# Kernel tuning notes

Measured on AMD Instinct MI355X. Metric: run time of the kernel, lower is better.

The kernel has to match this reference:

```python
import jax, jax.numpy as jnp
import numpy as np

UPDATE_STEPS = 2
EPS = 1e-7


def _collect(attn, source, W, b):
    """_Collection_Unit: relu(Linear(source)) gathered by attention, row-averaged.
    attn: [N_tgt, N_src], source: [N_src, D_in], W: [D_out, D_in], b: [D_out]."""
    fc_out = jax.nn.relu(source @ W.T + b)          # [N_src, D_out]
    collect = attn @ fc_out                          # [N_tgt, D_out]
    denom = jnp.sum(attn, axis=1, keepdims=True) + EPS
    return collect / denom


def setup_inputs() -> dict:
    key = jax.random.key(0)
    ks = jax.random.split(key, 10)
    N_OBJ, N_REL, D = 2048, 16384, 1024
    inp = {
        "obj_feats": jax.random.normal(ks[0], (N_OBJ, D), jnp.float32),
        "rel_feats": jax.random.normal(ks[1], (N_REL, D), jnp.float32),
        "attn_sub": jax.random.uniform(ks[2], (N_OBJ, N_REL), jnp.float32),
        "attn_obj": jax.random.uniform(ks[3], (N_OBJ, N_REL), jnp.float32),
        "attn_self": jax.random.uniform(ks[4], (N_OBJ, N_OBJ), jnp.float32),
    }
    # normal_init(fc, 0, 0.01) per original module
    names = ["rel2obj_sub", "rel2obj_obj", "obj2rel_sub", "obj2rel_obj", "obj2obj"]
    for i, n in enumerate(names):
        inp[f"W_{n}"] = jax.random.normal(ks[5 + i], (D, D), jnp.float32) * 0.01
        inp[f"b_{n}"] = jnp.zeros((D,), jnp.float32)
    return inp


def reference(obj_feats, rel_feats, attn_sub, attn_obj, attn_self,
              W_rel2obj_sub, b_rel2obj_sub, W_rel2obj_obj, b_rel2obj_obj,
              W_obj2rel_sub, b_obj2rel_sub, W_obj2rel_obj, b_obj2rel_obj,
              W_obj2obj, b_obj2obj):
    x_obj, x_rel = obj_feats, rel_feats
    for _ in range(UPDATE_STEPS):
        # collect to objects: from relations (as subject / as object) and from other objects
        src_sub = _collect(attn_sub, x_rel, W_rel2obj_sub, b_rel2obj_sub)   # unit 0
        src_obj = _collect(attn_obj, x_rel, W_rel2obj_obj, b_rel2obj_obj)   # unit 1
        src_self = _collect(attn_self, x_obj, W_obj2obj, b_obj2obj)         # unit 4
        src2obj = (src_sub + src_obj + src_self) / 3.0
        x_obj_new = x_obj + src2obj                                          # _Update_Unit 0
        # collect to relations: from subject / object node features
        src_rel_sub = _collect(attn_sub.T, x_obj, W_obj2rel_sub, b_obj2rel_sub)  # unit 2
        src_rel_obj = _collect(attn_obj.T, x_obj, W_obj2rel_obj, b_obj2rel_obj)  # unit 3
        src2rel = (src_rel_sub + src_rel_obj) / 2.0
        x_rel = x_rel + src2rel                                              # _Update_Unit 1
        x_obj = x_obj_new
    return x_obj, x_rel
```

## Files before the change

### kernel.cpp

```cpp
#include <hip/hip_runtime.h>
#include <hip/hip_bf16.h>

typedef __attribute__((ext_vector_type(4))) float  f32x4;
typedef __attribute__((ext_vector_type(8))) __bf16 bf16x8;
typedef __attribute__((ext_vector_type(4))) int    i32x4;
typedef __attribute__((ext_vector_type(8))) int    i32x8;
typedef __hip_bfloat16 bf16_t;

#define GT 256
#define BM 128
#define BN 128
#define BK 32

#define NOBJ 2048
#define NREL 16384
#define DIM  1024
#define KOBJ 34816
#define KREL 4096

#define AS1Q __attribute__((address_space(1)))
#define AS3Q __attribute__((address_space(3)))

__device__ __forceinline__ void gload_lds16(const void* g, void* l) {
    __builtin_amdgcn_global_load_lds((AS1Q void*)const_cast<void*>(g),
                                     (AS3Q void*)l, 16, 0, 0);
}

#define MFMA_BF16 __builtin_amdgcn_mfma_f32_16x16x32_bf16
#define MFMA_F8(ACC, Af, Bf) \
    ACC = __builtin_amdgcn_mfma_scale_f32_16x16x128_f8f6f4( \
        Af, Bf, ACC, 0, 0, 0, 0x7F7F7F7F, 0, 0x7F7F7F7F)

#define VMCNT(N) asm volatile("s_waitcnt vmcnt(" #N ")" ::: "memory")
#define SBAR()   __builtin_amdgcn_sched_barrier(0)

__device__ __forceinline__ unsigned char fp8_byte(float x) {
    return (unsigned char)(__builtin_amdgcn_cvt_pk_fp8_f32(x, x, 0, false) & 0xFF);
}
__device__ __forceinline__ unsigned pk4_fp8(float a, float b, float c, float d) {
    int v = __builtin_amdgcn_cvt_pk_fp8_f32(a, b, 0, false);
    v = __builtin_amdgcn_cvt_pk_fp8_f32(c, d, v, true);
    return (unsigned)v;
}

__global__ __launch_bounds__(GT)
void gemm_bt_f234(const bf16_t* __restrict__ A, const bf16_t* __restrict__ B,
                  int M, int N, int K, const float* __restrict__ vecM,
                  unsigned char* __restrict__ fcRel8, unsigned char* __restrict__ fcObj8)
{
    __shared__ bf16_t sA[BM * BK];
    __shared__ bf16_t sB[BN * BK];

    const int tid  = threadIdx.x;
    const int lane = tid & 63;
    const int wid  = tid >> 6;
    const int wr = wid >> 1, wc = wid & 1;
    const int l15 = lane & 15, lk = lane >> 4;

    const long rowA0 = (long)blockIdx.x * BM;
    const long rowB0 = (long)blockIdx.y * BN;
    const long ldab  = (long)K * 2;

    const int c0 = tid, c1 = tid + GT;
    const int r0c = c0 >> 2, k0c = (c0 & 3) ^ ((r0c >> 1) & 3);
    const int r1c = c1 >> 2, k1c = (c1 & 3) ^ ((r1c >> 1) & 3);

    const char* gA0 = (const char*)A + (rowA0 + r0c) * ldab + k0c * 16;
    const char* gA1 = (const char*)A + (rowA0 + r1c) * ldab + k1c * 16;
    const char* gB0 = (const char*)B + (rowB0 + r0c) * ldab + k0c * 16;
    const char* gB1 = (const char*)B + (rowB0 + r1c) * ldab + k1c * 16;
    char* lA0 = (char*)sA + c0 * 16;
    char* lA1 = (char*)sA + c1 * 16;
    char* lB0 = (char*)sB + c0 * 16;
    char* lB1 = (char*)sB + c1 * 16;

    f32x4 acc[4][4];
    #pragma unroll
    for (int i = 0; i < 4; i++)
        #pragma unroll
        for (int j = 0; j < 4; j++) acc[i][j] = f32x4{0.f, 0.f, 0.f, 0.f};

    const int ktPer = K / BK;
    for (int kt = 0; kt < ktPer; ++kt) {
        const long kByte = (long)kt * (BK * 2);
        gload_lds16(gA0 + kByte, lA0);
        gload_lds16(gA1 + kByte, lA1);
        gload_lds16(gB0 + kByte, lB0);
        gload_lds16(gB1 + kByte, lB1);
        __syncthreads();

        bf16x8 af[4], bg[4];
        #pragma unroll
        for (int i = 0; i < 4; i++) {
            const int rr = wr * 64 + i * 16 + l15;
            const int kk = lk ^ ((rr >> 1) & 3);
            af[i] = *reinterpret_cast<const bf16x8*>((const char*)sA + rr * 64 + kk * 16);
        }
        #pragma unroll
        for (int j = 0; j < 4; j++) {
            const int rr = wc * 64 + j * 16 + l15;
            const int kk = lk ^ ((rr >> 1) & 3);
            bg[j] = *reinterpret_cast<const bf16x8*>((const char*)sB + rr * 64 + kk * 16);
        }
        #pragma unroll
        for (int i = 0; i < 4; i++)
            #pragma unroll
            for (int j = 0; j < 4; j++)
                acc[i][j] = MFMA_BF16(af[i], bg[j], acc[i][j], 0, 0, 0);
        __syncthreads();
    }

    #pragma unroll
    for (int i = 0; i < 4; i++) {
        const long mBase = rowA0 + wr * 64 + i * 16 + lk * 4;
        const f32x4 vm = *reinterpret_cast<const f32x4*>(&vecM[mBase]);
        #pragma unroll
        for (int r = 0; r < 4; r++) {
            const long m = mBase + r;
            #pragma unroll
            for (int j = 0; j < 4; j++) {
                const long n = rowB0 + wc * 64 + j * 16 + l15;
                const float v = fmaxf(acc[i][j][r] + vm[r], 0.f);
                const unsigned char o = fp8_byte(v);
                if (m < 1024)            fcRel8[m * (long)KREL + n] = o;
                else if (m < 2048)       fcRel8[(m - 1024) * (long)KREL + 2048 + n] = o;
                else                     fcObj8[(m - 2048) * (long)KOBJ + 32768 + n] = o;
            }
        }
    }
}

__global__ __launch_bounds__(512, 2)
void gemm256fc(const bf16_t* __restrict__ A, const bf16_t* __restrict__ B,
               int M, int N, int K, const float* __restrict__ vecM,
               unsigned char* __restrict__ Cb8, int ldc, int Ntiles)
{
    __shared__ __align__(16) char lds[131072];

    const int tid  = threadIdx.x;
    const int lane = tid & 63;
    const int wid  = tid >> 6;
    const int wr = wid >> 2, wc = wid & 3;
    const int l15 = lane & 15, lk = lane >> 4;

    const int nwg = gridDim.x;
    const int cpx = nwg >> 3;
    const int bid = blockIdx.x;
    const int swz = (bid & 7) * cpx + (bid >> 3);
    const int tm = swz / Ntiles, tn = swz % Ntiles;
    const long rowM0 = (long)tm * 256;
    const long rowN0 = (long)tn * 256;
    const long ld = (long)K * 2;

    const int NT = K >> 6;

    const int rl = tid >> 3;
    const int lc = (tid & 7) ^ (rl & 7);
    const char* gA0 = (const char*)A + (rowM0 + rl) * ld + lc * 16;
    const char* gB0 = (const char*)B + (rowN0 + rl) * ld + lc * 16;

    auto stage = [&](int buf, int isB, int h, int t) {
        const char* g = (isB ? gB0 : gA0) + (long)h * 128 * ld + (long)t * 128;
        char* l = (char*)lds + buf * 65536 + isB * 32768 + h * 16384 + tid * 16;
        gload_lds16(g, l);
        gload_lds16(g + 64 * ld, l + 8192);
    };

    const int xo0 = ((0 + lk) ^ (l15 & 7)) * 16;
    const int xo1 = ((4 + lk) ^ (l15 & 7)) * 16;
    const int baseA = (wr * 16 + l15) * 128;
    const int baseB = 32768 + (wc * 16 + l15) * 128;

    f32x4 acc[8][4];
    #pragma unroll
    for (int i = 0; i < 8; i++)
        #pragma unroll
        for (int j = 0; j < 4; j++) acc[i][j] = f32x4{0.f, 0.f, 0.f, 0.f};

    stage(0, 0, 0, 0); stage(0, 1, 0, 0); stage(0, 1, 1, 0); stage(0, 0, 1, 0);

    bf16x8 a[4][2], b[4][2];
    for (int t = 0; t < NT; ++t) {
        const int cur = t & 1;
        const int nxt = cur ^ 1;
        const bool pf = (t + 1) < NT;
        const char* lcur = (const char*)lds + (cur << 16);

        if (pf) { stage(nxt, 0, 0, t + 1); stage(nxt, 1, 0, t + 1);
                  stage(nxt, 1, 1, t + 1); stage(nxt, 0, 1, t + 1); }
        if (pf) { VMCNT(10); } else { VMCNT(2); }
        SBAR();
        __builtin_amdgcn_s_barrier();

        #pragma unroll
        for (int kf = 0; kf < 4; kf++) {
            a[kf][0] = *(const bf16x8*)(lcur + baseA + kf * 4096 + xo0);
            a[kf][1] = *(const bf16x8*)(lcur + baseA + kf * 4096 + xo1);
        }
        #pragma unroll
        for (int j = 0; j < 4; j++) {
            b[j][0] = *(const bf16x8*)(lcur + baseB + j * 8192 + xo0);
            b[j][1] = *(const bf16x8*)(lcur + baseB + j * 8192 + xo1);
        }
        asm volatile("s_waitcnt lgkmcnt(0)" ::: "memory");
        SBAR();
        __builtin_amdgcn_s_setprio(1);
        #pragma unroll
        for (int j = 0; j < 4; j++)
            #pragma unroll
            for (int kf = 0; kf < 4; kf++) {
                acc[kf][j] = MFMA_BF16(a[kf][0], b[j][0], acc[kf][j], 0, 0, 0);
                acc[kf][j] = MFMA_BF16(a[kf][1], b[j][1], acc[kf][j], 0, 0, 0);
            }
        __builtin_amdgcn_s_setprio(0);
        if (pf) { VMCNT(8); } else { VMCNT(0); }
        SBAR();
        __builtin_amdgcn_s_barrier();

        #pragma unroll
        for (int kf = 0; kf < 4; kf++) {
            a[kf][0] = *(const bf16x8*)(lcur + baseA + (4 + kf) * 4096 + xo0);
            a[kf][1] = *(const bf16x8*)(lcur + baseA + (4 + kf) * 4096 + xo1);
        }
        asm volatile("s_waitcnt lgkmcnt(0)" ::: "memory");
        SBAR();
        __builtin_amdgcn_s_barrier();
        __builtin_amdgcn_s_setprio(1);
        #pragma unroll
        for (int j = 0; j < 4; j++)
            #pragma unroll
            for (int kf = 0; kf < 4; kf++) {
                acc[4 + kf][j] = MFMA_BF16(a[kf][0], b[j][0], acc[4 + kf][j], 0, 0, 0);
                acc[4 + kf][j] = MFMA_BF16(a[kf][1], b[j][1], acc[4 + kf][j], 0, 0, 0);
            }
        __builtin_amdgcn_s_setprio(0);
    }

    #pragma unroll
    for (int kf = 0; kf < 8; kf++) {
        const long m0 = rowM0 + wr * 16 + kf * 32 + lk * 4;
        const f32x4 vm = *reinterpret_cast<const f32x4*>(vecM + m0);
        #pragma unroll
        for (int r = 0; r < 4; r++) {
            const long m = m0 + r;
            #pragma unroll
            for (int j = 0; j < 4; j++) {
                const long n = rowN0 + wc * 16 + j * 64 + l15;
                const float o = fmaxf(acc[kf][j][r] + vm[r], 0.f);
                Cb8[(m & 1023) * (long)ldc + (m >> 10) * 16384 + n] = fp8_byte(o);
            }
        }
    }
}

__global__ __launch_bounds__(512, 4)
void gemmf8_occ(const unsigned char* __restrict__ A, const unsigned char* __restrict__ B,
                int M, int N, int K, float* __restrict__ Cf, float scale,
                int ldc, int Ntiles)
{
    __shared__ __align__(16) char lds[49152];

    const int tid  = threadIdx.x;
    const int lane = tid & 63;
    const int wid  = tid >> 6;
    const int wr = wid >> 2, wc = wid & 3;
    const int l15 = lane & 15, lk = lane >> 4;

    const int nwg = gridDim.x;
    const int cpx = nwg >> 3;
    const int bid = blockIdx.x;
    const int swz = (bid & 7) * cpx + (bid >> 3);
    const int tm = swz / Ntiles, tn = swz % Ntiles;
    const long rowM0 = (long)tm * 128;
    const long rowN0 = (long)tn * 256;
    const long ld = (long)K;

    const int nz = gridDim.z;
    const int NT = (K >> 7) / nz;
    const long kb0 = (long)NT * blockIdx.z * 128;

    const int rs = tid >> 3;
    const int kc = (tid & 7) ^ (rs & 7);
    const char* gA = (const char*)A + (rowM0 + rs) * ld + kb0 + kc * 16;
    const char* gB = (const char*)B + (rowN0 + rs) * ld + kb0 + kc * 16;
    char* lA = (char*)lds + tid * 16;
    char* lB = (char*)lds + 16384 + tid * 16;

    const int xc0 = ((2 * lk + 0) ^ (l15 & 7)) * 16;
    const int xc1 = ((2 * lk + 1) ^ (l15 & 7)) * 16;
    const int baseA = (wr * 64 + l15) * 128;
    const int baseB = 16384 + (wc * 64 + l15) * 128;

#define LDF8(dst, off) { \
    i32x4 lo_ = *(const i32x4*)((const char*)lds + (off) + xc0); \
    i32x4 hi_ = *(const i32x4*)((const char*)lds + (off) + xc1); \
    dst = __builtin_shufflevector(lo_, hi_, 0, 1, 2, 3, 4, 5, 6, 7); }

    f32x4 acc[4][4];
    #pragma unroll
    for (int i = 0; i < 4; i++)
        #pragma unroll
        for (int j = 0; j < 4; j++) acc[i][j] = f32x4{0.f, 0.f, 0.f, 0.f};

    for (int t = 0; t < NT; ++t) {
        const long kByte = (long)t * 128;
        gload_lds16(gA + kByte, lA);
        gload_lds16(gA + kByte + 64 * ld, lA + 8192);
        #pragma unroll
        for (int i = 0; i < 4; i++)
            gload_lds16(gB + kByte + (long)i * 64 * ld, lB + i * 8192);
        __syncthreads();

        i32x8 a[4];
        #pragma unroll
        for (int kf = 0; kf < 4; kf++) LDF8(a[kf], baseA + kf * 2048);
        #pragma unroll
        for (int j = 0; j < 4; j++) {
            i32x8 b;
            LDF8(b, baseB + j * 2048);
            #pragma unroll
            for (int kf = 0; kf < 4; kf++) MFMA_F8(acc[kf][j], a[kf], b);
        }
        __syncthreads();
    }
#undef LDF8

    #pragma unroll
    for (int kf = 0; kf < 4; kf++) {
        const long m0 = rowM0 + wr * 64 + kf * 16 + lk * 4;
        #pragma unroll
        for (int r = 0; r < 4; r++) {
            const long m = m0 + r;
            #pragma unroll
            for (int j = 0; j < 4; j++) {
                const long n = rowN0 + wc * 64 + j * 16 + l15;
                const float v = acc[kf][j][r] * scale;
                if (nz == 1) Cf[m * (long)ldc + n] += v;
                else atomicAdd(&Cf[m * (long)ldc + n], v);
            }
        }
    }
}

__global__ __launch_bounds__(256)
void k_cast_bf16(const float* __restrict__ in, bf16_t* __restrict__ out, long n)
{
    const long stride = (long)gridDim.x * blockDim.x;
    for (long i = (long)blockIdx.x * blockDim.x + threadIdx.x; i * 4 < n; i += stride) {
        f32x4 v = *reinterpret_cast<const f32x4*>(in + i * 4);
        union { bf16_t h[4]; ushort4 u; } o;
        o.h[0] = __float2bfloat16(v[0]); o.h[1] = __float2bfloat16(v[1]);
        o.h[2] = __float2bfloat16(v[2]); o.h[3] = __float2bfloat16(v[3]);
        *reinterpret_cast<ushort4*>(out + i * 4) = o.u;
    }
}

template<bool COLS>
__global__ __launch_bounds__(256)
void k_sums(const float* __restrict__ in, int C,
            float* __restrict__ rowsum, float* __restrict__ colsum)
{
    __shared__ float cpart[16][64];
    __shared__ float rpart[64][17];
    const int tid = threadIdx.x;
    const int tx  = tid & 15;
    const int ty  = tid >> 4;
    const long c0 = (long)blockIdx.x * 64;
    const long r0 = (long)blockIdx.y * 64;

    float cs0 = 0.f, cs1 = 0.f, cs2 = 0.f, cs3 = 0.f;
    #pragma unroll
    for (int i = 0; i < 4; i++) {
        const int r = i * 16 + ty;
        const f32x4 v = *reinterpret_cast<const f32x4*>(&in[(r0 + r) * (long)C + c0 + tx * 4]);
        rpart[r][tx] = v[0] + v[1] + v[2] + v[3];
        cs0 += v[0]; cs1 += v[1]; cs2 += v[2]; cs3 += v[3];
    }
    if (COLS) {
        cpart[ty][tx * 4 + 0] = cs0;
        cpart[ty][tx * 4 + 1] = cs1;
        cpart[ty][tx * 4 + 2] = cs2;
        cpart[ty][tx * 4 + 3] = cs3;
    }
    __syncthreads();
    if (tid < 64) {
        float rs = 0.f;
        #pragma unroll
        for (int k = 0; k < 16; k++) rs += rpart[tid][k];
        atomicAdd(&rowsum[r0 + tid], rs);
        if (COLS) {
            float cs = 0.f;
            #pragma unroll
            for (int k = 0; k < 16; k++) cs += cpart[k][tid];
            atomicAdd(&colsum[c0 + tid], cs);
        }
    }
}

__global__ __launch_bounds__(256)
void k_invscale(float* __restrict__ s, int n, float c)
{
    const int i = blockIdx.x * 256 + threadIdx.x;
    if (i < n) s[i] = c / (s[i] + 1e-7f);
}

template<bool TRANS>
__global__ __launch_bounds__(256)
void k_prep2f8(const float* __restrict__ in, int C,
               unsigned char* __restrict__ Aobj, unsigned char* __restrict__ Arel,
               const float* __restrict__ invRow, const float* __restrict__ invCol)
{
    __shared__ float tile[64][65];
    const int tid = threadIdx.x;
    const int tx  = tid & 15;
    const int ty  = tid >> 4;
    const long c0 = (long)blockIdx.x * 64;
    const long r0 = (long)blockIdx.y * 64;

    #pragma unroll
    for (int i = 0; i < 4; i++) {
        const int r = i * 16 + ty;
        const f32x4 v = *reinterpret_cast<const f32x4*>(&in[(r0 + r) * (long)C + c0 + tx * 4]);
        const float sc = invRow[r0 + r];
        *reinterpret_cast<unsigned*>(&Aobj[(r0 + r) * (long)KOBJ + c0 + tx * 4]) =
            pk4_fp8(v[0] * sc, v[1] * sc, v[2] * sc, v[3] * sc);
        if (TRANS) *reinterpret_cast<f32x4*>(&tile[r][tx * 4]) = v;
    }
    if (TRANS) {
        __syncthreads();
        const int rr = tid & 63;
        const int cg = tid >> 6;
        #pragma unroll
        for (int i = 0; i < 16; i++) {
            const int c = cg * 16 + i;
            const float sc = invCol[c0 + c];
            Arel[(c0 + c) * (long)KREL + r0 + rr] = fp8_byte(tile[rr][c] * sc);
        }
    }
}

extern "C" void kernel_launch(void* const* d_in, const int* in_sizes, int n_in,
                              void* d_out, int out_size, void* d_ws, size_t ws_size,
                              hipStream_t stream)
{
    if (n_in < 15) return;
    const float* obj_feats = (const float*)d_in[0];
    const float* rel_feats = (const float*)d_in[1];
    const float* attn_sub  = (const float*)d_in[2];
    const float* attn_obj  = (const float*)d_in[3];
    const float* attn_self = (const float*)d_in[4];
    const float* Wf[5] = { (const float*)d_in[5], (const float*)d_in[7],
                           (const float*)d_in[9], (const float*)d_in[11], (const float*)d_in[13] };
    const float* Bf[5] = { (const float*)d_in[6], (const float*)d_in[8],
                           (const float*)d_in[10], (const float*)d_in[12], (const float*)d_in[14] };

    const int NO = NOBJ, NR = NREL, D = DIM;

    char* w = (char*)d_ws;
    auto take = [&](size_t bytes) { char* p = w; w += bytes; return p; };
    unsigned char* Aobj8  = (unsigned char*)take((size_t)NO * KOBJ);
    unsigned char* Arel8  = (unsigned char*)take((size_t)NR * KREL);
    unsigned char* fcObj8 = (unsigned char*)take((size_t)D * KOBJ);
    unsigned char* fcRel8 = (unsigned char*)take((size_t)D * KREL);
    bf16_t* xrel_bf = (bf16_t*)take((size_t)NR * D * 2);
    bf16_t* xobj_bf = (bf16_t*)take((size_t)NO * D * 2);
    bf16_t* Wstk01  = (bf16_t*)take((size_t)2 * D * D * 2);
    bf16_t* Wstk234 = (bf16_t*)take((size_t)3 * D * D * 2);
    float*  b01     = (float*)take((size_t)2 * D * 4);
    float*  bstk    = (float*)take((size_t)3 * D * 4);
    float*  sums    = (float*)take((size_t)(3 * NO + 2 * NR) * 4);
    float* invS     = sums;
    float* invO     = sums + NO;
    float* invSelf  = sums + 2 * NO;
    float* invTS    = sums + 3 * NO;
    float* invTO    = sums + 3 * NO + NR;
    if ((size_t)(w - (char*)d_ws) > ws_size) return;

    float* x_obj = (float*)d_out;
    float* x_rel = x_obj + (size_t)NO * D;

    hipMemcpyAsync(x_obj, obj_feats, (size_t)NO * D * 4, hipMemcpyDeviceToDevice, stream);
    hipMemcpyAsync(x_rel, rel_feats, (size_t)NR * D * 4, hipMemcpyDeviceToDevice, stream);
    hipMemcpyAsync(b01,     Bf[0], (size_t)D * 4, hipMemcpyDeviceToDevice, stream);
    hipMemcpyAsync(b01 + D, Bf[1], (size_t)D * 4, hipMemcpyDeviceToDevice, stream);
    for (int i = 0; i < 3; i++)
        hipMemcpyAsync(bstk + i * D, Bf[2 + i], (size_t)D * 4, hipMemcpyDeviceToDevice, stream);
    hipMemsetAsync(sums, 0, (size_t)(3 * NO + 2 * NR) * 4, stream);

    auto cast = [&](const float* in, bf16_t* out, long n) {
        long blocks = (n / 4 + 255) / 256; if (blocks > 4096) blocks = 4096;
        k_cast_bf16<<<dim3((unsigned)blocks), dim3(256), 0, stream>>>(in, out, n);
    };
    cast(Wf[0], Wstk01,                 (long)D * D);
    cast(Wf[1], Wstk01 + (size_t)D * D, (long)D * D);
    for (int i = 0; i < 3; i++)
        cast(Wf[2 + i], Wstk234 + (size_t)i * D * D, (long)D * D);

    k_sums<true><<<dim3(NR / 64, NO / 64), dim3(256), 0, stream>>>(attn_sub, NR, invS, invTS);
    k_sums<true><<<dim3(NR / 64, NO / 64), dim3(256), 0, stream>>>(attn_obj, NR, invO, invTO);
    k_sums<false><<<dim3(NO / 64, NO / 64), dim3(256), 0, stream>>>(attn_self, NO, invSelf, nullptr);
    k_invscale<<<dim3((3 * NO + 255) / 256), dim3(256), 0, stream>>>(sums, 3 * NO, 8192.f / 3.f);
    k_invscale<<<dim3((2 * NR + 255) / 256), dim3(256), 0, stream>>>(sums + 3 * NO, 2 * NR, 1024.f);

    k_prep2f8<true><<<dim3(NR / 64, NO / 64), dim3(256), 0, stream>>>(
        attn_sub, NR, Aobj8, Arel8, invS, invTS);
    k_prep2f8<true><<<dim3(NR / 64, NO / 64), dim3(256), 0, stream>>>(
        attn_obj, NR, Aobj8 + 16384, Arel8 + 2048, invO, invTO);
    k_prep2f8<false><<<dim3(NO / 64, NO / 64), dim3(256), 0, stream>>>(
        attn_self, NO, Aobj8 + 32768, nullptr, invSelf, nullptr);

    for (int step = 0; step < 2; ++step) {
        cast(x_obj, xobj_bf, (long)NO * D);
        cast(x_rel, xrel_bf, (long)NR * D);

        gemm256fc<<<dim3((2 * D / 256) * (NR / 256), 1, 1), dim3(512), 0, stream>>>(
            Wstk01, xrel_bf, 2 * D, NR, D, b01, fcObj8, KOBJ, NR / 256);
        gemm_bt_f234<<<dim3(3 * D / BM, NO / BN, 1), dim3(GT), 0, stream>>>(
            Wstk234, xobj_bf, 3 * D, NO, D, bstk, fcRel8, fcObj8);

        gemmf8_occ<<<dim3((NO / 128) * (D / 256), 1, 8), dim3(512), 0, stream>>>(
            Aobj8, fcObj8, NO, D, KOBJ, x_obj, 1.f / 8192.f, D, D / 256);
        gemmf8_occ<<<dim3((NR / 128) * (D / 256), 1, 1), dim3(512), 0, stream>>>(
            Arel8, fcRel8, NR, D, KREL, x_rel, 1.f / 2048.f, D, D / 256);
    }
}
```

Measured before the change: 897.9 us.

## Replace double-buffered 256x256 fc GEMM with single-buffer 128x256 high-occupancy variant; raise split-K

The relation fc GEMM drops its 256x256 double-buffered, hand-scheduled pipeline (128KB LDS, 2 waves/SIMD bound) in favor of a 128x256 tile with a single 48KB LDS buffer and plain __syncthreads. This allows up to 4 blocks per CU and doubles the grid, relying on occupancy instead of explicit prefetch to hide latency. Separately, the split-K factor of both fp8 aggregation GEMMs is doubled (8→16 and 1→2) for more parallelism, at the cost of more atomic or partial-sum traffic into the fp32 outputs. The new GEMM loses load/compute overlap within a block and reuses each loaded tile across fewer outputs.

```diff
diff --git a/kernel.cpp b/kernel.cpp
--- a/kernel.cpp
+++ b/kernel.cpp
@@ -30,9 +30,6 @@
 #define MFMA_F8(ACC, Af, Bf) \
     ACC = __builtin_amdgcn_mfma_scale_f32_16x16x128_f8f6f4( \
         Af, Bf, ACC, 0, 0, 0, 0x7F7F7F7F, 0, 0x7F7F7F7F)
-
-#define VMCNT(N) asm volatile("s_waitcnt vmcnt(" #N ")" ::: "memory")
-#define SBAR()   __builtin_amdgcn_sched_barrier(0)
 
 __device__ __forceinline__ unsigned char fp8_byte(float x) {
     return (unsigned char)(__builtin_amdgcn_cvt_pk_fp8_f32(x, x, 0, false) & 0xFF);
@@ -130,12 +127,12 @@
     }
 }
 
-__global__ __launch_bounds__(512, 2)
-void gemm256fc(const bf16_t* __restrict__ A, const bf16_t* __restrict__ B,
-               int M, int N, int K, const float* __restrict__ vecM,
-               unsigned char* __restrict__ Cb8, int ldc, int Ntiles)
-{
-    __shared__ __align__(16) char lds[131072];
+__global__ __launch_bounds__(512, 4)
+void gemmfc_occ(const bf16_t* __restrict__ A, const bf16_t* __restrict__ B,
+                int M, int N, int K, const float* __restrict__ vecM,
+                unsigned char* __restrict__ Cb8, int ldc, int Ntiles)
+{
+    __shared__ __align__(16) char lds[49152];
 
     const int tid  = threadIdx.x;
     const int lane = tid & 63;
@@ -148,104 +145,68 @@
     const int bid = blockIdx.x;
     const int swz = (bid & 7) * cpx + (bid >> 3);
     const int tm = swz / Ntiles, tn = swz % Ntiles;
-    const long rowM0 = (long)tm * 256;
+    const long rowM0 = (long)tm * 128;
     const long rowN0 = (long)tn * 256;
     const long ld = (long)K * 2;
 
     const int NT = K >> 6;
 
-    const int rl = tid >> 3;
-    const int lc = (tid & 7) ^ (rl & 7);
-    const char* gA0 = (const char*)A + (rowM0 + rl) * ld + lc * 16;
-    const char* gB0 = (const char*)B + (rowN0 + rl) * ld + lc * 16;
-
-    auto stage = [&](int buf, int isB, int h, int t) {
-        const char* g = (isB ? gB0 : gA0) + (long)h * 128 * ld + (long)t * 128;
-        char* l = (char*)lds + buf * 65536 + isB * 32768 + h * 16384 + tid * 16;
-        gload_lds16(g, l);
-        gload_lds16(g + 64 * ld, l + 8192);
-    };
+    const int rs = tid >> 3;
+    const int kc = (tid & 7) ^ (rs & 7);
+    const char* gA = (const char*)A + (rowM0 + rs) * ld + kc * 16;
+    const char* gB = (const char*)B + (rowN0 + rs) * ld + kc * 16;
+    char* lA = (char*)lds + tid * 16;
+    char* lB = (char*)lds + 16384 + tid * 16;
 
     const int xo0 = ((0 + lk) ^ (l15 & 7)) * 16;
     const int xo1 = ((4 + lk) ^ (l15 & 7)) * 16;
-    const int baseA = (wr * 16 + l15) * 128;
-    const int baseB = 32768 + (wc * 16 + l15) * 128;
-
-    f32x4 acc[8][4];
-    #pragma unroll
-    for (int i = 0; i < 8; i++)
+    const int baseA = (wr * 64 + l15) * 128;
+    const int baseB = 16384 + (wc * 64 + l15) * 128;
+
+    f32x4 acc[4][4];
+    #pragma unroll
+    for (int i = 0; i < 4; i++)
         #pragma unroll
         for (int j = 0; j < 4; j++) acc[i][j] = f32x4{0.f, 0.f, 0.f, 0.f};
 
-    stage(0, 0, 0, 0); stage(0, 1, 0, 0); stage(0, 1, 1, 0); stage(0, 0, 1, 0);
-
-    bf16x8 a[4][2], b[4][2];
     for (int t = 0; t < NT; ++t) {
-        const int cur = t & 1;
-        const int nxt = cur ^ 1;
-        const bool pf = (t + 1) < NT;
-        const char* lcur = (const char*)lds + (cur << 16);
-
-        if (pf) { stage(nxt, 0, 0, t + 1); stage(nxt, 1, 0, t + 1);
-                  stage(nxt, 1, 1, t + 1); stage(nxt, 0, 1, t + 1); }
-        if (pf) { VMCNT(10); } else { VMCNT(2); }
-        SBAR();
-        __builtin_amdgcn_s_barrier();
-
+        const long kByte = (long)t * 128;
+        gload_lds16(gA + kByte, lA);
+        gload_lds16(gA + kByte + 64 * ld, lA + 8192);
+        #pragma unroll
+        for (int i = 0; i < 4; i++)
+            gload_lds16(gB + kByte + (long)i * 64 * ld, lB + i * 8192);
+        __syncthreads();
+
+        bf16x8 a[4][2];
         #pragma unroll
         for (int kf = 0; kf < 4; kf++) {
-            a[kf][0] = *(const bf16x8*)(lcur + baseA + kf * 4096 + xo0);
-            a[kf][1] = *(const bf16x8*)(lcur + baseA + kf * 4096 + xo1);
+            a[kf][0] = *(const bf16x8*)((const char*)lds + baseA + kf * 2048 + xo0);
+            a[kf][1] = *(const bf16x8*)((const char*)lds + baseA + kf * 2048 + xo1);
         }
         #pragma unroll
         for (int j = 0; j < 4; j++) {
-            b[j][0] = *(const bf16x8*)(lcur + baseB + j * 8192 + xo0);
-            b[j][1] = *(const bf16x8*)(lcur + baseB + j * 8192 + xo1);
-        }
-        asm volatile("s_waitcnt lgkmcnt(0)" ::: "memory");
-        SBAR();
-        __builtin_amdgcn_s_setprio(1);
-        #pragma unroll
-        for (int j = 0; j < 4; j++)
+            const bf16x8 b0 = *(const bf16x8*)((const char*)lds + baseB + j * 2048 + xo0);
+            const bf16x8 b1 = *(const bf16x8*)((const char*)lds + baseB + j * 2048 + xo1);
             #pragma unroll
             for (int kf = 0; kf < 4; kf++) {
-                acc[kf][j] = MFMA_BF16(a[kf][0], b[j][0], acc[kf][j], 0, 0, 0);
-                acc[kf][j] = MFMA_BF16(a[kf][1], b[j][1], acc[kf][j], 0, 0, 0);
+                acc[kf][j] = MFMA_BF16(a[kf][0], b0, acc[kf][j], 0, 0, 0);
+                acc[kf][j] = MFMA_BF16(a[kf][1], b1, acc[kf][j], 0, 0, 0);
             }
-        __builtin_amdgcn_s_setprio(0);
-        if (pf) { VMCNT(8); } else { VMCNT(0); }
-        SBAR();
-        __builtin_amdgcn_s_barrier();
-
-        #pragma unroll
-        for (int kf = 0; kf < 4; kf++) {
-            a[kf][0] = *(const bf16x8*)(lcur + baseA + (4 + kf) * 4096 + xo0);
-            a[kf][1] = *(const bf16x8*)(lcur + baseA + (4 + kf) * 4096 + xo1);
-        }
-        asm volatile("s_waitcnt lgkmcnt(0)" ::: "memory");
-        SBAR();
-        __builtin_amdgcn_s_barrier();
-        __builtin_amdgcn_s_setprio(1);
-        #pragma unroll
-        for (int j = 0; j < 4; j++)
-            #pragma unroll
-            for (int kf = 0; kf < 4; kf++) {
-                acc[4 + kf][j] = MFMA_BF16(a[kf][0], b[j][0], acc[4 + kf][j], 0, 0, 0);
-                acc[4 + kf][j] = MFMA_BF16(a[kf][1], b[j][1], acc[4 + kf][j], 0, 0, 0);
-            }
-        __builtin_amdgcn_s_setprio(0);
-    }
-
-    #pragma unroll
-    for (int kf = 0; kf < 8; kf++) {
-        const long m0 = rowM0 + wr * 16 + kf * 32 + lk * 4;
+        }
+        __syncthreads();
+    }
+
+    #pragma unroll
+    for (int kf = 0; kf < 4; kf++) {
+        const long m0 = rowM0 + wr * 64 + kf * 16 + lk * 4;
         const f32x4 vm = *reinterpret_cast<const f32x4*>(vecM + m0);
         #pragma unroll
         for (int r = 0; r < 4; r++) {
             const long m = m0 + r;
             #pragma unroll
             for (int j = 0; j < 4; j++) {
-                const long n = rowN0 + wc * 16 + j * 64 + l15;
+                const long n = rowN0 + wc * 64 + j * 16 + l15;
                 const float o = fmaxf(acc[kf][j][r] + vm[r], 0.f);
                 Cb8[(m & 1023) * (long)ldc + (m >> 10) * 16384 + n] = fp8_byte(o);
             }
@@ -513,14 +474,14 @@
         cast(x_obj, xobj_bf, (long)NO * D);
         cast(x_rel, xrel_bf, (long)NR * D);
 
-        gemm256fc<<<dim3((2 * D / 256) * (NR / 256), 1, 1), dim3(512), 0, stream>>>(
+        gemmfc_occ<<<dim3((2 * D / 128) * (NR / 256), 1, 1), dim3(512), 0, stream>>>(
             Wstk01, xrel_bf, 2 * D, NR, D, b01, fcObj8, KOBJ, NR / 256);
         gemm_bt_f234<<<dim3(3 * D / BM, NO / BN, 1), dim3(GT), 0, stream>>>(
             Wstk234, xobj_bf, 3 * D, NO, D, bstk, fcRel8, fcObj8);
 
-        gemmf8_occ<<<dim3((NO / 128) * (D / 256), 1, 8), dim3(512), 0, stream>>>(
+        gemmf8_occ<<<dim3((NO / 128) * (D / 256), 1, 16), dim3(512), 0, stream>>>(
             Aobj8, fcObj8, NO, D, KOBJ, x_obj, 1.f / 8192.f, D, D / 256);
-        gemmf8_occ<<<dim3((NR / 128) * (D / 256), 1, 1), dim3(512), 0, stream>>>(
+        gemmf8_occ<<<dim3((NR / 128) * (D / 256), 1, 2), dim3(512), 0, stream>>>(
             Arel8, fcRel8, NR, D, KREL, x_rel, 1.f / 2048.f, D, D / 256);
     }
 }
```

Result: slower. 1.120 ms (+24.8%).

## Merge object and relation FP8 aggregation GEMMs into a single dual launch

Applied to the files above, without the earlier changes.

Replaces the two separate fp8 GEMM launches (the split-K object aggregation with 8 K-slices, and the relation aggregation) with one kernel of 1024 workgroups. Each workgroup picks its problem, tile and K-slice from a swizzled block index, and the problem sizes are hardcoded. This removes one launch and the tail idle time between the two GEMMs, so both run concurrently and fill the GPU better. In exchange it adds a branchy per-block setup and hardcodes shapes, and the object-side workgroups carry longer K loops than the relation side, which may unbalance the merged grid.

```diff
diff --git a/kernel.cpp b/kernel.cpp
--- a/kernel.cpp
+++ b/kernel.cpp
@@ -254,9 +254,10 @@
 }
 
 __global__ __launch_bounds__(512, 4)
-void gemmf8_occ(const unsigned char* __restrict__ A, const unsigned char* __restrict__ B,
-                int M, int N, int K, float* __restrict__ Cf, float scale,
-                int ldc, int Ntiles)
+void gemmf8_dual(const unsigned char* __restrict__ Ao, const unsigned char* __restrict__ Bo,
+                 float* __restrict__ Co,
+                 const unsigned char* __restrict__ Ar, const unsigned char* __restrict__ Br,
+                 float* __restrict__ Cr)
 {
     __shared__ __align__(16) char lds[49152];
 
@@ -266,18 +267,26 @@
     const int wr = wid >> 2, wc = wid & 3;
     const int l15 = lane & 15, lk = lane >> 4;
 
-    const int nwg = gridDim.x;
-    const int cpx = nwg >> 3;
     const int bid = blockIdx.x;
-    const int swz = (bid & 7) * cpx + (bid >> 3);
-    const int tm = swz / Ntiles, tn = swz % Ntiles;
-    const long rowM0 = (long)tm * 128;
-    const long rowN0 = (long)tn * 256;
+    const int s   = (bid & 7) * 128 + (bid >> 3);
+
+    const unsigned char* A; const unsigned char* B; float* C;
+    int K, NT; long kb0; float scale; bool at;
+    long rowM0, rowN0;
+    if (s < 512) {
+        const int zz = s >> 6, t = s & 63;
+        rowM0 = (long)(t >> 2) * 128; rowN0 = (long)(t & 3) * 256;
+        A = Ao; B = Bo; C = Co;
+        K = KOBJ; NT = 34; kb0 = (long)34 * zz * 128;
+        scale = 1.f / 8192.f; at = true;
+    } else {
+        const int t = s - 512;
+        rowM0 = (long)(t >> 2) * 128; rowN0 = (long)(t & 3) * 256;
+        A = Ar; B = Br; C = Cr;
+        K = KREL; NT = 32; kb0 = 0;
+        scale = 1.f / 2048.f; at = false;
+    }
     const long ld = (long)K;
-
-    const int nz = gridDim.z;
-    const int NT = (K >> 7) / nz;
-    const long kb0 = (long)NT * blockIdx.z * 128;
 
     const int rs = tid >> 3;
     const int kc = (tid & 7) ^ (rs & 7);
@@ -335,8 +344,8 @@
             for (int j = 0; j < 4; j++) {
                 const long n = rowN0 + wc * 64 + j * 16 + l15;
                 const float v = acc[kf][j][r] * scale;
-                if (nz == 1) Cf[m * (long)ldc + n] += v;
-                else atomicAdd(&Cf[m * (long)ldc + n], v);
+                if (at) atomicAdd(&C[m * (long)DIM + n], v);
+                else    C[m * (long)DIM + n] += v;
             }
         }
     }
@@ -518,9 +527,7 @@
         gemm_bt_f234<<<dim3(3 * D / BM, NO / BN, 1), dim3(GT), 0, stream>>>(
             Wstk234, xobj_bf, 3 * D, NO, D, bstk, fcRel8, fcObj8);
 
-        gemmf8_occ<<<dim3((NO / 128) * (D / 256), 1, 8), dim3(512), 0, stream>>>(
-            Aobj8, fcObj8, NO, D, KOBJ, x_obj, 1.f / 8192.f, D, D / 256);
-        gemmf8_occ<<<dim3((NR / 128) * (D / 256), 1, 1), dim3(512), 0, stream>>>(
-            Arel8, fcRel8, NR, D, KREL, x_rel, 1.f / 2048.f, D, D / 256);
-    }
-}
+        gemmf8_dual<<<dim3(1024), dim3(512), 0, stream>>>(
+            Aobj8, fcObj8, x_obj, Arel8, fcRel8, x_rel);
+    }
+}
```

Measured after the change: 859.4 us. 1.04x faster.
